# Optimization experiments

Measured on AMD Instinct MI355X. Metric: run time of the kernel, lower is better.

## Reference

```python
import jax, jax.numpy as jnp
import numpy as np

EMBED_DIM = 512
NUM_HEADS = 8
B, L_Q, L_K = 2, 2048, 2048


def setup_inputs() -> dict:
    key = jax.random.key(0)
    ks = jax.random.split(key, 8)
    s = 0.02  # weight init scale
    return {
        "query": jax.random.normal(ks[0], (B, L_Q, EMBED_DIM), jnp.float32),
        "key":   jax.random.normal(ks[1], (B, L_K, EMBED_DIM), jnp.float32),
        "value": jax.random.normal(ks[2], (B, L_K, EMBED_DIM), jnp.float32),
        "wq": jax.random.normal(ks[3], (EMBED_DIM, EMBED_DIM), jnp.float32) * s,
        "wk": jax.random.normal(ks[4], (EMBED_DIM, EMBED_DIM), jnp.float32) * s,
        "wv": jax.random.normal(ks[5], (EMBED_DIM, EMBED_DIM), jnp.float32) * s,
        "bq": jnp.zeros((EMBED_DIM,), jnp.float32),
        "bk": jnp.zeros((EMBED_DIM,), jnp.float32),
        "bv": jnp.zeros((EMBED_DIM,), jnp.float32),
        "wo": jax.random.normal(ks[6], (EMBED_DIM, EMBED_DIM), jnp.float32) * s,
        "bo": jnp.zeros((EMBED_DIM,), jnp.float32),
    }


def _prob_sparse_mask(query, key, num_heads):
    # Faithful to _prob_QK: max-mean sparsity score, top-k query selection,
    # gather of reduced queries, reduced QK matmul (vectorized, no python loops).
    Bq, Lq, D = query.shape
    Lk = key.shape[1]
    dh = D // num_heads
    n_top = int(np.log(Lk))  # int(np.ceil/np.log) as in source forward: int(np.log(L_K))
    Q = query.reshape(Bq, Lq, num_heads, dh)
    K = key.reshape(Bq, Lk, num_heads, dh)
    Qh = jnp.transpose(Q, (0, 2, 1, 3))                      # [B,H,Lq,dh]
    # NOTE: source does K.transpose(1,2).reshape(B,H,D,L_K) -- a reshape, not a
    # transpose of the last two dims. We replicate that exactly.
    Kr = jnp.transpose(K, (0, 2, 1, 3)).reshape(Bq, num_heads, dh, Lk)  # [B,H,dh,Lk]
    QK = jnp.einsum('bhqd,bhdk->bhqk', Qh, Kr)               # [B,H,Lq,Lk]
    M = QK.max(-1) - QK.sum(-1) / Lk                         # max-mean score [B,H,Lq]
    _, M_top = jax.lax.top_k(M, n_top)                       # [B,H,n_top]
    Q_red = jnp.take_along_axis(Qh, M_top[..., None], axis=2)  # [B,H,n_top,dh]
    QK_red = jnp.einsum('bhtd,bhdk->bhtk', Q_red, Kr)        # [B,H,n_top,Lk]
    # Scatter reduced rows back into a full additive attn mask (zeros elsewhere).
    mask = jnp.zeros((Bq, num_heads, Lq, Lk), QK.dtype)
    bi = jnp.arange(Bq)[:, None, None]
    hi = jnp.arange(num_heads)[None, :, None]
    return mask.at[bi, hi, M_top].set(QK_red)


def reference(query, key, value, wq, wk, wv, bq, bk, bv, wo, bo):
    Bq, Lq, D = query.shape
    Lk = key.shape[1]
    H = NUM_HEADS
    dh = D // H
    mask = _prob_sparse_mask(query, key, H)                  # [B,H,Lq,Lk]
    q = (query @ wq.T + bq).reshape(Bq, Lq, H, dh).transpose(0, 2, 1, 3)
    k = (key @ wk.T + bk).reshape(Bq, Lk, H, dh).transpose(0, 2, 1, 3)
    v = (value @ wv.T + bv).reshape(Bq, Lk, H, dh).transpose(0, 2, 1, 3)
    scores = jnp.einsum('bhqd,bhkd->bhqk', q, k) * (dh ** -0.5) + mask
    attn = jax.nn.softmax(scores, axis=-1)                   # dropout inactive (eval)
    out = jnp.einsum('bhqk,bhkd->bhqd', attn, v)
    out = out.transpose(0, 2, 1, 3).reshape(Bq, Lq, D)
    return out @ wo.T + bo
```

## Files before the change

kernel.cpp:

```cpp
#include <hip/hip_runtime.h>
#include <type_traits>

#define DEV static __device__ __forceinline__

typedef short s16;
typedef __attribute__((ext_vector_type(4))) short short4_t;
typedef __attribute__((ext_vector_type(8))) short short8;
typedef __attribute__((ext_vector_type(4))) float f32x4;

#define NB 2
#define NH 8
#define SL 2048
#define DM 512
#define DH 64
#define NTOP 7
#define LOG2E 1.4426950408889634f
#define NROWS (NB*NH*SL)
#define FSPLIT 4
#define SSPLIT 4

DEV short f2bf(float x){
  union { float f; unsigned u; } v; v.f = x;
  unsigned r = v.u + 0x7fffu + ((v.u >> 16) & 1u);
  return (short)(r >> 16);
}
DEV float bf2f(short b){
  union { float f; unsigned u; } v; v.u = ((unsigned)(unsigned short)b) << 16;
  return v.f;
}
DEV f32x4 mfma16(short8 a, short8 b, f32x4 c){
  return __builtin_amdgcn_mfma_f32_16x16x32_bf16(a, b, c, 0, 0, 0);
}
DEV unsigned cvtpk(float lo, float hi){
  unsigned r;
  asm("v_cvt_pk_bf16_f32 %0, %1, %2" : "=v"(r) : "v"(lo), "v"(hi));
  return r;
}
DEV void gl2lds16(const s16* g, s16* l){
  __builtin_amdgcn_global_load_lds(
      (const __attribute__((address_space(1))) unsigned*)g,
      (__attribute__((address_space(3))) unsigned*)l, 16, 0, 0);
}

__global__ void prep_kernel(const float* __restrict__ query, const float* __restrict__ key,
    const float* __restrict__ value,
    const float* __restrict__ wq, const float* __restrict__ wk,
    const float* __restrict__ wv, const float* __restrict__ wo,
    s16* __restrict__ q_hi, s16* __restrict__ q_lo, s16* __restrict__ xk, s16* __restrict__ xv,
    s16* __restrict__ khi, s16* __restrict__ klo,
    s16* __restrict__ wqb, s16* __restrict__ wkb, s16* __restrict__ wvb, s16* __restrict__ wob){
  const int nbb = (NB*SL*DM)/256;
  const int wbb = (DM*DM)/256;
  __shared__ s16 thi[64][66];
  __shared__ s16 tlo[64][66];
  int bid = blockIdx.x;
  int t = threadIdx.x;
  if (bid < nbb){
    int i = bid*256 + t;
    float v = query[i];
    short h = f2bf(v);
    q_hi[i] = h;
    q_lo[i] = f2bf(v - bf2f(h));
    return;
  }
  bid -= nbb;
  if (bid < nbb){ int i = bid*256 + t; xk[i] = f2bf(key[i]); return; }
  bid -= nbb;
  if (bid < nbb){ int i = bid*256 + t; xv[i] = f2bf(value[i]); return; }
  bid -= nbb;
  if (bid < 512){
    int k6 = bid & 31, h = (bid >> 5) & 7, b = bid >> 8;
    int kl = t & 63, dq = t >> 6;
    #pragma unroll
    for (int dd = 0; dd < 16; ++dd){
      int d = dd*4 + dq;
      float v = key[((size_t)b*SL + d*32 + k6)*DM + h*DH + kl];
      short hh = f2bf(v);
      thi[d][kl] = hh;
      tlo[d][kl] = f2bf(v - bf2f(hh));
    }
    __syncthreads();
    int d2 = t & 63, kq = t >> 6;
    size_t obase = (((size_t)(b*NH + h))*SL + (size_t)k6*64)*DH;
    #pragma unroll
    for (int kk = 0; kk < 16; ++kk){
      int kl2 = kk*4 + kq;
      khi[obase + (size_t)kl2*DH + d2] = thi[d2][kl2];
      klo[obase + (size_t)kl2*DH + d2] = tlo[d2][kl2];
    }
    return;
  }
  bid -= 512;
  if (bid < wbb){ int i = bid*256 + t; wqb[i] = f2bf(wq[i]); return; }
  bid -= wbb;
  if (bid < wbb){ int i = bid*256 + t; wkb[i] = f2bf(wk[i]); return; }
  bid -= wbb;
  if (bid < wbb){ int i = bid*256 + t; wvb[i] = f2bf(wv[i]); return; }
  bid -= wbb;
  if (bid < wbb){ int i = bid*256 + t; wob[i] = f2bf(wo[i]); return; }
}

__global__ __launch_bounds__(256) void vpt_kernel(const s16* __restrict__ Vp, s16* __restrict__ VpT){
  __shared__ s16 tl[64][66];
  int bid = blockIdx.x;
  int k6 = bid & 31, h = (bid >> 5) & 7, b = bid >> 8;
  int t = threadIdx.x;
  int d = t & 63, kq = t >> 6;
  #pragma unroll
  for (int kk = 0; kk < 16; ++kk){
    int kl = kk*4 + kq;
    tl[kl][d] = Vp[((size_t)b*SL + k6*64 + kl)*DM + h*DH + d];
  }
  __syncthreads();
  int kl2 = t & 63, dq = t >> 6;
  int kp = (kl2 & 32) + ((kl2 >> 2) & 3)*8 + (kl2 & 3) + ((kl2 >> 4) & 1)*4;
  size_t obase = ((size_t)(b*NH + h))*DH*SL + (size_t)k6*64;
  #pragma unroll
  for (int dd = 0; dd < 16; ++dd){
    int d2 = dd*4 + dq;
    VpT[obase + (size_t)d2*SL + kp] = tl[kl2][d2];
  }
}

template<int OUTF32>
DEV void gemm_body(const s16* __restrict__ A, const s16* __restrict__ Bw,
        const float* __restrict__ bias, void* __restrict__ Cout, int bid, int tid, float scale){
  __shared__ __align__(16) s16 Abuf[2][128*64];
  __shared__ __align__(16) s16 Bbuf[2][64*64];
  int nt = bid >> 3, ot = bid & 7;
  int w = tid >> 6, l = tid & 63;
  int lr = l & 15, lg = l >> 4;
  int n0 = nt*128, o0 = ot*64;
  auto stage = [&](int cur, int kg){
    #pragma unroll
    for (int i = 0; i < 4; ++i){
      int r = w*32 + i*8 + (l>>3);
      int cs = (l&7) ^ (r&7);
      gl2lds16(A + (size_t)(n0 + r)*DM + kg + cs*8, &Abuf[cur][(w*32 + i*8)*64]);
    }
    #pragma unroll
    for (int i = 0; i < 2; ++i){
      int r = w*16 + i*8 + (l>>3);
      int cs = (l&7) ^ (r&7);
      gl2lds16(Bw + (size_t)(o0 + r)*DM + kg + cs*8, &Bbuf[cur][(w*16 + i*8)*64]);
    }
  };
  f32x4 acc[2][4] = {};
  stage(0, 0);
  __syncthreads();
  const int NIT = DM/64;
  for (int it = 0; it < NIT; ++it){
    int cur = it & 1;
    if (it + 1 < NIT) stage(cur^1, (it+1)*64);
    #pragma unroll
    for (int kc = 0; kc < 2; ++kc){
      short8 a0 = *(const short8*)&Abuf[cur][(w*32 +      lr)*64 + ((kc*4+lg) ^ (lr&7))*8];
      short8 a1 = *(const short8*)&Abuf[cur][(w*32 + 16 + lr)*64 + ((kc*4+lg) ^ (lr&7))*8];
      #pragma unroll
      for (int c = 0; c < 4; ++c){
        short8 bf = *(const short8*)&Bbuf[cur][(c*16 + lr)*64 + ((kc*4+lg) ^ (lr&7))*8];
        acc[0][c] = mfma16(a0, bf, acc[0][c]);
        acc[1][c] = mfma16(a1, bf, acc[1][c]);
      }
    }
    __syncthreads();
  }
  #pragma unroll
  for (int sub = 0; sub < 2; ++sub)
    #pragma unroll
    for (int c = 0; c < 4; ++c){
      int col = o0 + c*16 + lr;
      float bb = bias[col];
      #pragma unroll
      for (int j = 0; j < 4; ++j){
        int row = n0 + w*32 + sub*16 + lg*4 + j;
        float v = (acc[sub][c][j] + bb)*scale;
        if (OUTF32) ((float*)Cout)[(size_t)row*DM + col] = v;
        else        ((s16*) Cout)[(size_t)row*DM + col] = f2bf(v);
      }
    }
}

__global__ __launch_bounds__(256) void gemm_proj(const s16* __restrict__ Aq, const s16* __restrict__ Ak,
        const s16* __restrict__ Av, const s16* __restrict__ Wq, const s16* __restrict__ Wk,
        const s16* __restrict__ Wv, const float* __restrict__ bq, const float* __restrict__ bk,
        const float* __restrict__ bv, s16* __restrict__ Oq, s16* __restrict__ Ok, s16* __restrict__ Ov){
  int which = blockIdx.x >> 8;
  const s16* A  = which == 0 ? Aq : which == 1 ? Ak : Av;
  const s16* Bw = which == 0 ? Wq : which == 1 ? Wk : Wv;
  const float* bias = which == 0 ? bq : which == 1 ? bk : bv;
  s16* C = which == 0 ? Oq : which == 1 ? Ok : Ov;
  float scale = which == 0 ? 0.125f*LOG2E : 1.0f;
  gemm_body<0>(A, Bw, bias, C, blockIdx.x & 255, threadIdx.x, scale);
}

__global__ __launch_bounds__(256) void gemm_out(const s16* __restrict__ A, const s16* __restrict__ Bw,
        const float* __restrict__ bias, float* __restrict__ Cout){
  gemm_body<1>(A, Bw, bias, Cout, blockIdx.x, threadIdx.x, 1.0f);
}

__global__ __launch_bounds__(512) void stats_kernel(const s16* __restrict__ qhi, const s16* __restrict__ qlo,
        const s16* __restrict__ khi, const s16* __restrict__ klo,
        float* __restrict__ Mmx, float* __restrict__ Msm){
  __shared__ __align__(16) s16 Hbuf[2][64*64];
  __shared__ __align__(16) s16 Lbuf[2][64*64];
  int bid = blockIdx.x;
  int s = bid & 3, qt = (bid >> 2) & 15, h = (bid >> 6) & 7, b = bid >> 9;
  int tid = threadIdx.x;
  int w = tid >> 6, l = tid & 63;
  int lr = l & 15, lg = l >> 4;
  int dx = lr & 7;
  int q0 = qt*128 + w*16;
  const s16* qp  = qhi + ((size_t)b*SL + q0 + lr)*DM + h*DH + lg*8;
  const s16* qlp = qlo + ((size_t)b*SL + q0 + lr)*DM + h*DH + lg*8;
  short8 qh0 = *(const short8*)qp;
  short8 qh1 = *(const short8*)(qp + 32);
  short8 ql0 = *(const short8*)qlp;
  short8 ql1 = *(const short8*)(qlp + 32);
  const s16* kb  = khi + ((size_t)b*NH + h)*SL*DH;
  const s16* klb = klo + ((size_t)b*NH + h)*SL*DH;
  const s16* hR0 = &Hbuf[0][lr*64 + ((lg      ^ dx)*8)];
  const s16* hR1 = &Hbuf[0][lr*64 + (((4+lg) ^ dx)*8)];
  const s16* lR0 = &Lbuf[0][lr*64 + ((lg      ^ dx)*8)];
  const s16* lR1 = &Lbuf[0][lr*64 + (((4+lg) ^ dx)*8)];
  int rS = tid >> 3;
  int csK = (tid & 7) ^ (rS & 7);
  auto stage = [&](int cur, int kg){
    gl2lds16(kb  + (size_t)(kg + rS)*DH + csK*8, &Hbuf[cur][w*512]);
    gl2lds16(klb + (size_t)(kg + rS)*DH + csK*8, &Lbuf[cur][w*512]);
  };
  float mx = -1e30f, sm = 0.f;
  auto body = [&](auto CURC){
    constexpr int CUR = decltype(CURC)::value;
    #pragma unroll
    for (int t = 0; t < 4; ++t){
      short8 kh0 = *(const short8*)(hR0 + CUR*4096 + t*1024);
      short8 kh1 = *(const short8*)(hR1 + CUR*4096 + t*1024);
      short8 kl0 = *(const short8*)(lR0 + CUR*4096 + t*1024);
      short8 kl1 = *(const short8*)(lR1 + CUR*4096 + t*1024);
      f32x4 sacc = {};
      sacc = mfma16(kh0, qh0, sacc);
      sacc = mfma16(kh1, qh1, sacc);
      sacc = mfma16(kl0, qh0, sacc);
      sacc = mfma16(kl1, qh1, sacc);
      sacc = mfma16(kh0, ql0, sacc);
      sacc = mfma16(kh1, ql1, sacc);
      #pragma unroll
      for (int j = 0; j < 4; ++j){ mx = fmaxf(mx, sacc[j]); sm += sacc[j]; }
    }
  };
  int kbeg = s*(SL/SSPLIT);
  const int NI2 = (SL/SSPLIT)/128;
  stage(0, kbeg);
  __syncthreads();
  #pragma unroll 1
  for (int i2 = 0; i2 < NI2; ++i2){
    stage(1, kbeg + (2*i2+1)*64);
    body(std::integral_constant<int,0>{});
    __syncthreads();
    if (i2 < NI2-1) stage(0, kbeg + (2*i2+2)*64);
    body(std::integral_constant<int,1>{});
    __syncthreads();
  }
  mx = fmaxf(mx, __shfl_xor(mx, 16));
  mx = fmaxf(mx, __shfl_xor(mx, 32));
  sm += __shfl_xor(sm, 16);
  sm += __shfl_xor(sm, 32);
  if (lg == 0){
    size_t row = ((size_t)b*NH + h)*SL + q0 + lr;
    Mmx[(size_t)s*NROWS + row] = mx;
    Msm[(size_t)s*NROWS + row] = sm;
  }
}

__global__ __launch_bounds__(256) void topk_kernel(const float* __restrict__ Mmx,
        const float* __restrict__ Msm, int* __restrict__ topidx, int* __restrict__ rowsel){
  int bh = blockIdx.x;
  int t = threadIdx.x;
  int w = t >> 6, l = t & 63;
  __shared__ float smv[SL];
  __shared__ float rv[4];
  __shared__ int   ri[4];
  size_t base = (size_t)bh*SL;
  for (int i = t; i < SL; i += 256){
    float mx = Mmx[base + i];
    float sm = Msm[base + i];
    #pragma unroll
    for (int s = 1; s < SSPLIT; ++s){
      mx = fmaxf(mx, Mmx[(size_t)s*NROWS + base + i]);
      sm += Msm[(size_t)s*NROWS + base + i];
    }
    smv[i] = mx - sm*(1.0f/SL);
    rowsel[base + i] = -1;
  }
  __syncthreads();
  for (int tt = 0; tt < NTOP; ++tt){
    float bvv = -1e38f; int bi = SL;
    for (int i = t; i < SL; i += 256){
      float v = smv[i];
      if (v > bvv){ bvv = v; bi = i; }
    }
    #pragma unroll
    for (int off = 32; off >= 1; off >>= 1){
      float ov = __shfl_xor(bvv, off);
      int oi = __shfl_xor(bi, off);
      if (ov > bvv || (ov == bvv && oi < bi)){ bvv = ov; bi = oi; }
    }
    if (l == 0){ rv[w] = bvv; ri[w] = bi; }
    __syncthreads();
    if (t == 0){
      float bv2 = rv[0]; int bi2 = ri[0];
      #pragma unroll
      for (int ww = 1; ww < 4; ++ww)
        if (rv[ww] > bv2 || (rv[ww] == bv2 && ri[ww] < bi2)){ bv2 = rv[ww]; bi2 = ri[ww]; }
      topidx[bh*8 + tt] = bi2;
      rowsel[base + bi2] = tt;
      smv[bi2] = -1e38f;
    }
    __syncthreads();
  }
}

__global__ __launch_bounds__(256) void maskrow_kernel(const float* __restrict__ query,
        const float* __restrict__ key, const int* __restrict__ topidx, float* __restrict__ maskrows){
  __shared__ float tile[64][65];
  __shared__ float qs[NTOP][64];
  int bid = blockIdx.x;
  int k6 = bid & 31, h = (bid >> 5) & 7, b = bid >> 8;
  int bh = b*NH + h;
  int t = threadIdx.x;
  int kl = t & 63, w = t >> 6;
  for (int i = t; i < NTOP*64; i += 256){
    int tt = i >> 6, d = i & 63;
    qs[tt][d] = query[((size_t)b*SL + topidx[bh*8 + tt])*DM + h*DH + d];
  }
  #pragma unroll
  for (int dd = 0; dd < 16; ++dd){
    int d = dd*4 + w;
    tile[d][kl] = key[((size_t)b*SL + d*32 + k6)*DM + h*DH + kl];
  }
  __syncthreads();
  for (int tt = w; tt < NTOP; tt += 4){
    float acc = 0.f;
    #pragma unroll
    for (int d = 0; d < 64; ++d)
      acc = fmaf(qs[tt][d], tile[d][kl], acc);
    maskrows[((size_t)bh*NTOP + tt)*SL + k6*64 + kl] = acc*LOG2E;
  }
}

__global__ __launch_bounds__(512) void flash_kernel(const s16* __restrict__ Qp, const s16* __restrict__ Kp,
        const s16* __restrict__ VpT, const float* __restrict__ maskrows, const int* __restrict__ rowsel,
        float* __restrict__ Opart, float* __restrict__ lpart){
  __shared__ __align__(16) s16 Kbuf[2][64*64];
  __shared__ __align__(16) s16 Vbuf[2][64*64];
  int bid = blockIdx.x;
  int s = bid & 3, qt = (bid >> 2) & 15, h = (bid >> 6) & 7, b = bid >> 9;
  int tid = threadIdx.x;
  int w = tid >> 6, l = tid & 63;
  int lr = l & 15, lg = l >> 4;
  int dx = lr & 7;
  int q0 = qt*128 + w*16;
  int bh = b*NH + h;
  const s16* qp = Qp + ((size_t)b*SL + q0 + lr)*DM + h*DH + lg*8;
  short8 bq0 = *(const short8*)qp;
  short8 bq1 = *(const short8*)(qp + 32);
  int sel = rowsel[(size_t)bh*SL + q0 + lr];
  const float* mrow = maskrows + ((size_t)bh*NTOP + (sel >= 0 ? sel : 0))*SL;
  const s16* kpb = Kp + (size_t)b*SL*DM + h*DH;
  const s16* vtb = VpT + (size_t)bh*DH*SL;
  const s16* kR0 = &Kbuf[0][lr*64 + ((lg      ^ dx)*8)];
  const s16* kR1 = &Kbuf[0][lr*64 + (((4+lg) ^ dx)*8)];
  const s16* vR0 = &Vbuf[0][lr*64 + ((lg      ^ dx)*8)];
  const s16* vR1 = &Vbuf[0][lr*64 + (((4+lg) ^ dx)*8)];
  int rS = tid >> 3;
  int csK = (tid & 7) ^ (rS & 7);
  auto stage = [&](int cur, int kg){
    gl2lds16(kpb + (size_t)(kg + rS)*DM + csK*8, &Kbuf[cur][w*512]);
    gl2lds16(vtb + (size_t)rS*SL + kg + csK*8, &Vbuf[cur][w*512]);
  };
  f32x4 acc[4] = {};
  float ls0 = 0.f, ls1 = 0.f, ls2 = 0.f, ls3 = 0.f;
  auto body = [&](auto CURC, int k0){
    constexpr int CUR = decltype(CURC)::value;
    float pv[4][4];
    #pragma unroll
    for (int t = 0; t < 4; ++t){
      short8 ka0 = *(const short8*)(kR0 + CUR*4096 + t*1024);
      short8 ka1 = *(const short8*)(kR1 + CUR*4096 + t*1024);
      f32x4 sc = {};
      sc = mfma16(ka0, bq0, sc);
      sc = mfma16(ka1, bq1, sc);
      #pragma unroll
      for (int j = 0; j < 4; ++j) pv[t][j] = sc[j];
    }
    if (sel >= 0){
      #pragma unroll
      for (int t = 0; t < 4; ++t)
        #pragma unroll
        for (int j = 0; j < 4; ++j)
          pv[t][j] += mrow[k0 + t*16 + lg*4 + j];
    }
    #pragma unroll
    for (int t = 0; t < 4; ++t){
      pv[t][0] = exp2f(pv[t][0]); ls0 += pv[t][0];
      pv[t][1] = exp2f(pv[t][1]); ls1 += pv[t][1];
      pv[t][2] = exp2f(pv[t][2]); ls2 += pv[t][2];
      pv[t][3] = exp2f(pv[t][3]); ls3 += pv[t][3];
    }
    short8 paf[2];
    #pragma unroll
    for (int kt = 0; kt < 2; ++kt){
      union { unsigned u[4]; short8 s8; } uu;
      uu.u[0] = cvtpk(pv[2*kt][0],   pv[2*kt][1]);
      uu.u[1] = cvtpk(pv[2*kt][2],   pv[2*kt][3]);
      uu.u[2] = cvtpk(pv[2*kt+1][0], pv[2*kt+1][1]);
      uu.u[3] = cvtpk(pv[2*kt+1][2], pv[2*kt+1][3]);
      paf[kt] = uu.s8;
    }
    #pragma unroll
    for (int c = 0; c < 4; ++c){
      short8 vf0 = *(const short8*)(vR0 + CUR*4096 + c*1024);
      acc[c] = mfma16(vf0, paf[0], acc[c]);
      short8 vf1 = *(const short8*)(vR1 + CUR*4096 + c*1024);
      acc[c] = mfma16(vf1, paf[1], acc[c]);
    }
  };
  int kbeg = s*(SL/FSPLIT);
  const int NI2 = (SL/FSPLIT)/128;
  stage(0, kbeg);
  __syncthreads();
  #pragma unroll 1
  for (int i2 = 0; i2 < NI2; ++i2){
    stage(1, kbeg + (2*i2+1)*64);
    body(std::integral_constant<int,0>{}, kbeg + 2*i2*64);
    __syncthreads();
    if (i2 < NI2-1) stage(0, kbeg + (2*i2+2)*64);
    body(std::integral_constant<int,1>{}, kbeg + (2*i2+1)*64);
    __syncthreads();
  }
  float lsum = (ls0 + ls1) + (ls2 + ls3);
  lsum += __shfl_xor(lsum, 16);
  lsum += __shfl_xor(lsum, 32);
  size_t row = (size_t)bh*SL + q0 + lr;
  float* Op = Opart + ((size_t)s*NROWS + row)*DH;
  #pragma unroll
  for (int c = 0; c < 4; ++c)
    *(f32x4*)(Op + c*16 + lg*4) = acc[c];
  if (lg == 0)
    lpart[(size_t)s*NROWS + row] = lsum;
}

__global__ __launch_bounds__(256) void flash_combine(const float* __restrict__ Opart,
        const float* __restrict__ lpart, s16* __restrict__ outh){
  int row = blockIdx.x*4 + (threadIdx.x >> 6);
  int d = threadIdx.x & 63;
  float L = 0.f, o = 0.f;
  #pragma unroll
  for (int s = 0; s < FSPLIT; ++s){
    L += lpart[(size_t)s*NROWS + row];
    o += Opart[((size_t)s*NROWS + row)*DH + d];
  }
  o /= L;
  int b = row >> 14, h = (row >> 11) & 7, q = row & (SL - 1);
  outh[((size_t)b*SL + q)*DM + h*DH + d] = f2bf(o);
}

extern "C" void kernel_launch(void* const* d_in, const int* in_sizes, int n_in,
                              void* d_out, int out_size, void* d_ws, size_t ws_size,
                              hipStream_t stream){
  (void)in_sizes; (void)n_in; (void)out_size;
  const float* query = (const float*)d_in[0];
  const float* key   = (const float*)d_in[1];
  const float* value = (const float*)d_in[2];
  const float* wq    = (const float*)d_in[3];
  const float* wk    = (const float*)d_in[4];
  const float* wv    = (const float*)d_in[5];
  const float* bq    = (const float*)d_in[6];
  const float* bk    = (const float*)d_in[7];
  const float* bv    = (const float*)d_in[8];
  const float* wo    = (const float*)d_in[9];
  const float* bo    = (const float*)d_in[10];

  const size_t NE = (size_t)NB*SL*DM;
  const size_t WE = (size_t)DM*DM;

  char* p = (char*)d_ws;
  size_t off = 0;
  auto alloc = [&](size_t n)->char*{ char* r = p + off; off += (n + 255) & ~(size_t)255; return r; };
  s16* wob = (s16*)alloc(WE*2);
  s16* Qp  = (s16*)alloc(NE*2);
  s16* Kp  = (s16*)alloc(NE*2);
  s16* VpT = (s16*)alloc(NE*2);
  float* maskrows = (float*)alloc((size_t)NB*NH*NTOP*SL*4);
  int* topidx   = (int*)alloc((size_t)NB*NH*8*4);
  int* rowsel   = (int*)alloc((size_t)NROWS*4);
  float* Mmx    = (float*)alloc((size_t)SSPLIT*NROWS*4);
  float* Msm    = (float*)alloc((size_t)SSPLIT*NROWS*4);
  float* lpart  = (float*)alloc((size_t)FSPLIT*NROWS*4);
  float* Opart  = (float*)alloc((size_t)FSPLIT*NROWS*DH*4);
  s16* outh = (s16*)alloc(NE*2);
  s16* q_hi = (s16*)alloc(NE*2);
  s16* q_lo = (s16*)alloc(NE*2);
  s16* xk   = (s16*)alloc(NE*2);
  s16* xv   = (s16*)alloc(NE*2);
  s16* khatT_hi = (s16*)alloc(NE*2);
  s16* khatT_lo = (s16*)alloc(NE*2);
  s16* wqb = (s16*)alloc(WE*2);
  s16* wkb = (s16*)alloc(WE*2);
  s16* wvb = (s16*)alloc(WE*2);
  s16* Vp  = (s16*)alloc(NE*2);
  if (off > ws_size) return;

  const int nbb = (int)(NE/256);
  const int wbb = (int)(WE/256);
  prep_kernel<<<3*nbb + 512 + 4*wbb, 256, 0, stream>>>(query, key, value, wq, wk, wv, wo,
      q_hi, q_lo, xk, xv, khatT_hi, khatT_lo, wqb, wkb, wvb, wob);

  gemm_proj<<<3*256, 256, 0, stream>>>(q_hi, xk, xv, wqb, wkb, wvb, bq, bk, bv, Qp, Kp, Vp);
  vpt_kernel<<<512, 256, 0, stream>>>(Vp, VpT);

  stats_kernel<<<NB*NH*(SL/128)*SSPLIT, 512, 0, stream>>>(q_hi, q_lo, khatT_hi, khatT_lo, Mmx, Msm);
  topk_kernel<<<NB*NH, 256, 0, stream>>>(Mmx, Msm, topidx, rowsel);
  maskrow_kernel<<<512, 256, 0, stream>>>(query, key, topidx, maskrows);

  flash_kernel<<<NB*NH*(SL/128)*FSPLIT, 512, 0, stream>>>(Qp, Kp, VpT, maskrows, rowsel,
      Opart, lpart);
  flash_combine<<<NROWS/4, 256, 0, stream>>>(Opart, lpart, outh);
  gemm_out<<<256, 256, 0, stream>>>(outh, wob, bo, (float*)d_out);
}
```

Baseline: 141.3 us.

## Deepen K/V staging to a 4-buffer async pipeline with explicit vmcnt waits

Result: slower. 147.5 us (+4.4%).

```diff
diff --git a/kernel.cpp b/kernel.cpp
--- a/kernel.cpp
+++ b/kernel.cpp
@@ -18,6 +18,10 @@
 #define NROWS (NB*NH*SL)
 #define FSPLIT 4
 #define SSPLIT 4
+
+#define SCHEDB() __builtin_amdgcn_sched_barrier(0)
+#define WAITVM(N) do{ asm volatile("s_waitcnt vmcnt(" #N ")" ::: "memory"); SCHEDB(); }while(0)
+#define BAR() do{ __builtin_amdgcn_s_barrier(); SCHEDB(); }while(0)
 
 DEV short f2bf(float x){
   union { float f; unsigned u; } v; v.f = x;
@@ -202,8 +206,8 @@
 __global__ __launch_bounds__(512) void stats_kernel(const s16* __restrict__ qhi, const s16* __restrict__ qlo,
         const s16* __restrict__ khi, const s16* __restrict__ klo,
         float* __restrict__ Mmx, float* __restrict__ Msm){
-  __shared__ __align__(16) s16 Hbuf[2][64*64];
-  __shared__ __align__(16) s16 Lbuf[2][64*64];
+  __shared__ __align__(16) s16 Hbuf[4][64*64];
+  __shared__ __align__(16) s16 Lbuf[4][64*64];
   int bid = blockIdx.x;
   int s = bid & 3, qt = (bid >> 2) & 15, h = (bid >> 6) & 7, b = bid >> 9;
   int tid = threadIdx.x;
@@ -225,9 +229,10 @@
   const s16* lR1 = &Lbuf[0][lr*64 + (((4+lg) ^ dx)*8)];
   int rS = tid >> 3;
   int csK = (tid & 7) ^ (rS & 7);
-  auto stage = [&](int cur, int kg){
-    gl2lds16(kb  + (size_t)(kg + rS)*DH + csK*8, &Hbuf[cur][w*512]);
-    gl2lds16(klb + (size_t)(kg + rS)*DH + csK*8, &Lbuf[cur][w*512]);
+  int kbeg = s*(SL/SSPLIT);
+  auto stage = [&](int buf, int kg){
+    gl2lds16(kb  + (size_t)(kg + rS)*DH + csK*8, &Hbuf[buf][w*512]);
+    gl2lds16(klb + (size_t)(kg + rS)*DH + csK*8, &Lbuf[buf][w*512]);
   };
   float mx = -1e30f, sm = 0.f;
   auto body = [&](auto CURC){
@@ -249,19 +254,24 @@
       for (int j = 0; j < 4; ++j){ mx = fmaxf(mx, sacc[j]); sm += sacc[j]; }
     }
   };
-  int kbeg = s*(SL/SSPLIT);
-  const int NI2 = (SL/SSPLIT)/128;
-  stage(0, kbeg);
-  __syncthreads();
-  #pragma unroll 1
-  for (int i2 = 0; i2 < NI2; ++i2){
-    stage(1, kbeg + (2*i2+1)*64);
-    body(std::integral_constant<int,0>{});
-    __syncthreads();
-    if (i2 < NI2-1) stage(0, kbeg + (2*i2+2)*64);
-    body(std::integral_constant<int,1>{});
-    __syncthreads();
-  }
+  stage(0, kbeg); stage(1, kbeg + 64); stage(2, kbeg + 128);
+  auto step = [&](auto TC){
+    constexpr int T = decltype(TC)::value;
+    BAR();
+    if constexpr (T + 3 < 8) stage((T+3)&3, kbeg + (T+3)*64);
+    if constexpr (T <= 4) WAITVM(6);
+    else if constexpr (T == 5) WAITVM(4);
+    else if constexpr (T == 6) WAITVM(2);
+    else WAITVM(0);
+    BAR();
+    __builtin_amdgcn_s_setprio(1);
+    body(std::integral_constant<int, T&3>{});
+    __builtin_amdgcn_s_setprio(0);
+  };
+  step(std::integral_constant<int,0>{}); step(std::integral_constant<int,1>{});
+  step(std::integral_constant<int,2>{}); step(std::integral_constant<int,3>{});
+  step(std::integral_constant<int,4>{}); step(std::integral_constant<int,5>{});
+  step(std::integral_constant<int,6>{}); step(std::integral_constant<int,7>{});
   mx = fmaxf(mx, __shfl_xor(mx, 16));
   mx = fmaxf(mx, __shfl_xor(mx, 32));
   sm += __shfl_xor(sm, 16);
@@ -352,8 +362,8 @@
 __global__ __launch_bounds__(512) void flash_kernel(const s16* __restrict__ Qp, const s16* __restrict__ Kp,
         const s16* __restrict__ VpT, const float* __restrict__ maskrows, const int* __restrict__ rowsel,
         float* __restrict__ Opart, float* __restrict__ lpart){
-  __shared__ __align__(16) s16 Kbuf[2][64*64];
-  __shared__ __align__(16) s16 Vbuf[2][64*64];
+  __shared__ __align__(16) s16 Kbuf[4][64*64];
+  __shared__ __align__(16) s16 Vbuf[4][64*64];
   int bid = blockIdx.x;
   int s = bid & 3, qt = (bid >> 2) & 15, h = (bid >> 6) & 7, b = bid >> 9;
   int tid = threadIdx.x;
@@ -375,9 +385,10 @@
   const s16* vR1 = &Vbuf[0][lr*64 + (((4+lg) ^ dx)*8)];
   int rS = tid >> 3;
   int csK = (tid & 7) ^ (rS & 7);
-  auto stage = [&](int cur, int kg){
-    gl2lds16(kpb + (size_t)(kg + rS)*DM + csK*8, &Kbuf[cur][w*512]);
-    gl2lds16(vtb + (size_t)rS*SL + kg + csK*8, &Vbuf[cur][w*512]);
+  int kbeg = s*(SL/FSPLIT);
+  auto stage = [&](int buf, int kg){
+    gl2lds16(kpb + (size_t)(kg + rS)*DM + csK*8, &Kbuf[buf][w*512]);
+    gl2lds16(vtb + (size_t)rS*SL + kg + csK*8, &Vbuf[buf][w*512]);
   };
   f32x4 acc[4] = {};
   float ls0 = 0.f, ls1 = 0.f, ls2 = 0.f, ls3 = 0.f;
@@ -426,19 +437,24 @@
       acc[c] = mfma16(vf1, paf[1], acc[c]);
     }
   };
-  int kbeg = s*(SL/FSPLIT);
-  const int NI2 = (SL/FSPLIT)/128;
-  stage(0, kbeg);
-  __syncthreads();
-  #pragma unroll 1
-  for (int i2 = 0; i2 < NI2; ++i2){
-    stage(1, kbeg + (2*i2+1)*64);
-    body(std::integral_constant<int,0>{}, kbeg + 2*i2*64);
-    __syncthreads();
-    if (i2 < NI2-1) stage(0, kbeg + (2*i2+2)*64);
-    body(std::integral_constant<int,1>{}, kbeg + (2*i2+1)*64);
-    __syncthreads();
-  }
+  stage(0, kbeg); stage(1, kbeg + 64); stage(2, kbeg + 128);
+  auto step = [&](auto TC){
+    constexpr int T = decltype(TC)::value;
+    BAR();
+    if constexpr (T + 3 < 8) stage((T+3)&3, kbeg + (T+3)*64);
+    if constexpr (T <= 4) WAITVM(6);
+    else if constexpr (T == 5) WAITVM(4);
+    else if constexpr (T == 6) WAITVM(2);
+    else WAITVM(0);
+    BAR();
+    __builtin_amdgcn_s_setprio(1);
+    body(std::integral_constant<int, T&3>{}, kbeg + T*64);
+    __builtin_amdgcn_s_setprio(0);
+  };
+  step(std::integral_constant<int,0>{}); step(std::integral_constant<int,1>{});
+  step(std::integral_constant<int,2>{}); step(std::integral_constant<int,3>{});
+  step(std::integral_constant<int,4>{}); step(std::integral_constant<int,5>{});
+  step(std::integral_constant<int,6>{}); step(std::integral_constant<int,7>{});
   float lsum = (ls0 + ls1) + (ls2 + ls3);
   lsum += __shfl_xor(lsum, 16);
   lsum += __shfl_xor(lsum, 32);
```

## Switch flash attention to 32x32x16 MFMA with 4 waves of 32 rows

Applied to the files above, without the earlier changes.

Result: no change. 140.2 us (-0.7%).

```diff
diff --git a/kernel.cpp b/kernel.cpp
--- a/kernel.cpp
+++ b/kernel.cpp
@@ -7,6 +7,7 @@
 typedef __attribute__((ext_vector_type(4))) short short4_t;
 typedef __attribute__((ext_vector_type(8))) short short8;
 typedef __attribute__((ext_vector_type(4))) float f32x4;
+typedef __attribute__((ext_vector_type(16))) float f32x16;
 
 #define NB 2
 #define NH 8
@@ -30,6 +31,9 @@
 }
 DEV f32x4 mfma16(short8 a, short8 b, f32x4 c){
   return __builtin_amdgcn_mfma_f32_16x16x32_bf16(a, b, c, 0, 0, 0);
+}
+DEV f32x16 mfma32(short8 a, short8 b, f32x16 c){
+  return __builtin_amdgcn_mfma_f32_32x32x16_bf16(a, b, c, 0, 0, 0);
 }
 DEV unsigned cvtpk(float lo, float hi){
   unsigned r;
@@ -113,12 +117,11 @@
   }
   __syncthreads();
   int kl2 = t & 63, dq = t >> 6;
-  int kp = (kl2 & 32) + ((kl2 >> 2) & 3)*8 + (kl2 & 3) + ((kl2 >> 4) & 1)*4;
   size_t obase = ((size_t)(b*NH + h))*DH*SL + (size_t)k6*64;
   #pragma unroll
   for (int dd = 0; dd < 16; ++dd){
     int d2 = dd*4 + dq;
-    VpT[obase + (size_t)d2*SL + kp] = tl[kl2][d2];
+    VpT[obase + (size_t)d2*SL + kl2] = tl[kl2][d2];
   }
 }
 
@@ -349,82 +352,97 @@
   }
 }
 
-__global__ __launch_bounds__(512) void flash_kernel(const s16* __restrict__ Qp, const s16* __restrict__ Kp,
-        const s16* __restrict__ VpT, const float* __restrict__ maskrows, const int* __restrict__ rowsel,
+__global__ __launch_bounds__(256, 3) void flash_kernel(const s16* __restrict__ Qp,
+        const s16* __restrict__ Kp, const s16* __restrict__ VpT,
+        const float* __restrict__ maskrows, const int* __restrict__ rowsel,
         float* __restrict__ Opart, float* __restrict__ lpart){
-  __shared__ __align__(16) s16 Kbuf[2][64*64];
-  __shared__ __align__(16) s16 Vbuf[2][64*64];
+  __shared__ __align__(16) s16 SB[4*64*64];
   int bid = blockIdx.x;
   int s = bid & 3, qt = (bid >> 2) & 15, h = (bid >> 6) & 7, b = bid >> 9;
   int tid = threadIdx.x;
   int w = tid >> 6, l = tid & 63;
-  int lr = l & 15, lg = l >> 4;
-  int dx = lr & 7;
-  int q0 = qt*128 + w*16;
+  int ln = l & 31, lh = l >> 5;
+  int q0 = qt*128 + w*32;
   int bh = b*NH + h;
-  const s16* qp = Qp + ((size_t)b*SL + q0 + lr)*DM + h*DH + lg*8;
-  short8 bq0 = *(const short8*)qp;
-  short8 bq1 = *(const short8*)(qp + 32);
-  int sel = rowsel[(size_t)bh*SL + q0 + lr];
+  const s16* qp = Qp + ((size_t)b*SL + q0 + ln)*DM + h*DH + lh*8;
+  short8 bq[4];
+  #pragma unroll
+  for (int kc = 0; kc < 4; ++kc) bq[kc] = *(const short8*)(qp + kc*16);
+  int sel = rowsel[(size_t)bh*SL + q0 + ln];
   const float* mrow = maskrows + ((size_t)bh*NTOP + (sel >= 0 ? sel : 0))*SL;
   const s16* kpb = Kp + (size_t)b*SL*DM + h*DH;
   const s16* vtb = VpT + (size_t)bh*DH*SL;
-  const s16* kR0 = &Kbuf[0][lr*64 + ((lg      ^ dx)*8)];
-  const s16* kR1 = &Kbuf[0][lr*64 + (((4+lg) ^ dx)*8)];
-  const s16* vR0 = &Vbuf[0][lr*64 + ((lg      ^ dx)*8)];
-  const s16* vR1 = &Vbuf[0][lr*64 + (((4+lg) ^ dx)*8)];
-  int rS = tid >> 3;
-  int csK = (tid & 7) ^ (rS & 7);
+  const s16* kR[2][4];
+  #pragma unroll
+  for (int g = 0; g < 2; ++g)
+    #pragma unroll
+    for (int kc = 0; kc < 4; ++kc)
+      kR[g][kc] = &SB[(g*32 + ln)*64 + (((kc*2 + lh) ^ (ln & 7))*8)];
+  int rS8 = l >> 3;
+  int csS = (l & 7) ^ (rS8 & 7);
   auto stage = [&](int cur, int kg){
-    gl2lds16(kpb + (size_t)(kg + rS)*DM + csK*8, &Kbuf[cur][w*512]);
-    gl2lds16(vtb + (size_t)rS*SL + kg + csK*8, &Vbuf[cur][w*512]);
+    #pragma unroll
+    for (int c = 0; c < 2; ++c){
+      int r = c*32 + w*8 + rS8;
+      gl2lds16(kpb + (size_t)(kg + r)*DM + csS*8, &SB[(size_t)cur*4096 + (c*32 + w*8)*64]);
+      gl2lds16(vtb + (size_t)r*SL + kg + csS*8, &SB[8192 + (size_t)cur*4096 + (c*32 + w*8)*64]);
+    }
   };
-  f32x4 acc[4] = {};
+  f32x16 accO[2] = {};
   float ls0 = 0.f, ls1 = 0.f, ls2 = 0.f, ls3 = 0.f;
   auto body = [&](auto CURC, int k0){
-    constexpr int CUR = decltype(CURC)::value;
-    float pv[4][4];
-    #pragma unroll
-    for (int t = 0; t < 4; ++t){
-      short8 ka0 = *(const short8*)(kR0 + CUR*4096 + t*1024);
-      short8 ka1 = *(const short8*)(kR1 + CUR*4096 + t*1024);
-      f32x4 sc = {};
-      sc = mfma16(ka0, bq0, sc);
-      sc = mfma16(ka1, bq1, sc);
-      #pragma unroll
-      for (int j = 0; j < 4; ++j) pv[t][j] = sc[j];
-    }
+    constexpr int CB = decltype(CURC)::value * 8192;
+    f32x16 S[2] = {};
+    #pragma unroll
+    for (int g = 0; g < 2; ++g)
+      #pragma unroll
+      for (int kc = 0; kc < 4; ++kc){
+        short8 kf = *(const short8*)((const char*)kR[g][kc] + CB);
+        S[g] = mfma32(kf, bq[kc], S[g]);
+      }
     if (sel >= 0){
       #pragma unroll
-      for (int t = 0; t < 4; ++t)
+      for (int g = 0; g < 2; ++g)
         #pragma unroll
-        for (int j = 0; j < 4; ++j)
-          pv[t][j] += mrow[k0 + t*16 + lg*4 + j];
-    }
-    #pragma unroll
-    for (int t = 0; t < 4; ++t){
-      pv[t][0] = exp2f(pv[t][0]); ls0 += pv[t][0];
-      pv[t][1] = exp2f(pv[t][1]); ls1 += pv[t][1];
-      pv[t][2] = exp2f(pv[t][2]); ls2 += pv[t][2];
-      pv[t][3] = exp2f(pv[t][3]); ls3 += pv[t][3];
-    }
-    short8 paf[2];
-    #pragma unroll
-    for (int kt = 0; kt < 2; ++kt){
+        for (int rq = 0; rq < 4; ++rq)
+          #pragma unroll
+          for (int j = 0; j < 4; ++j)
+            S[g][rq*4 + j] += mrow[k0 + g*32 + rq*8 + lh*4 + j];
+    }
+    #pragma unroll
+    for (int g = 0; g < 2; ++g)
+      #pragma unroll
+      for (int rq = 0; rq < 4; ++rq){
+        S[g][rq*4+0] = exp2f(S[g][rq*4+0]); ls0 += S[g][rq*4+0];
+        S[g][rq*4+1] = exp2f(S[g][rq*4+1]); ls1 += S[g][rq*4+1];
+        S[g][rq*4+2] = exp2f(S[g][rq*4+2]); ls2 += S[g][rq*4+2];
+        S[g][rq*4+3] = exp2f(S[g][rq*4+3]); ls3 += S[g][rq*4+3];
+      }
+    unsigned W[2][8];
+    #pragma unroll
+    for (int g = 0; g < 2; ++g)
+      #pragma unroll
+      for (int t = 0; t < 8; ++t)
+        W[g][t] = cvtpk(S[g][2*t], S[g][2*t+1]);
+    short8 pf[4];
+    #pragma unroll
+    for (int kc = 0; kc < 4; ++kc){
+      int g = kc >> 1, j = kc & 1;
+      unsigned a0 = W[g][4*j + 0], a1 = W[g][4*j + 2];
+      asm("v_permlane32_swap_b32 %0, %1" : "+v"(a0), "+v"(a1));
+      unsigned b0 = W[g][4*j + 1], b1 = W[g][4*j + 3];
+      asm("v_permlane32_swap_b32 %0, %1" : "+v"(b0), "+v"(b1));
       union { unsigned u[4]; short8 s8; } uu;
-      uu.u[0] = cvtpk(pv[2*kt][0],   pv[2*kt][1]);
-      uu.u[1] = cvtpk(pv[2*kt][2],   pv[2*kt][3]);
-      uu.u[2] = cvtpk(pv[2*kt+1][0], pv[2*kt+1][1]);
-      uu.u[3] = cvtpk(pv[2*kt+1][2], pv[2*kt+1][3]);
-      paf[kt] = uu.s8;
-    }
-    #pragma unroll
-    for (int c = 0; c < 4; ++c){
-      short8 vf0 = *(const short8*)(vR0 + CUR*4096 + c*1024);
-      acc[c] = mfma16(vf0, paf[0], acc[c]);
-      short8 vf1 = *(const short8*)(vR1 + CUR*4096 + c*1024);
-      acc[c] = mfma16(vf1, paf[1], acc[c]);
-    }
+      uu.u[0] = a0; uu.u[1] = b0; uu.u[2] = a1; uu.u[3] = b1;
+      pf[kc] = uu.s8;
+    }
+    #pragma unroll
+    for (int dg = 0; dg < 2; ++dg)
+      #pragma unroll
+      for (int kc = 0; kc < 4; ++kc){
+        short8 vf = *(const short8*)((const char*)kR[dg][kc] + CB + 16384);
+        accO[dg] = mfma32(vf, pf[kc], accO[dg]);
+      }
   };
   int kbeg = s*(SL/FSPLIT);
   const int NI2 = (SL/FSPLIT)/128;
@@ -440,14 +458,17 @@
     __syncthreads();
   }
   float lsum = (ls0 + ls1) + (ls2 + ls3);
-  lsum += __shfl_xor(lsum, 16);
   lsum += __shfl_xor(lsum, 32);
-  size_t row = (size_t)bh*SL + q0 + lr;
+  size_t row = (size_t)bh*SL + q0 + ln;
   float* Op = Opart + ((size_t)s*NROWS + row)*DH;
   #pragma unroll
-  for (int c = 0; c < 4; ++c)
-    *(f32x4*)(Op + c*16 + lg*4) = acc[c];
-  if (lg == 0)
+  for (int dg = 0; dg < 2; ++dg)
+    #pragma unroll
+    for (int rq = 0; rq < 4; ++rq){
+      f32x4 v = { accO[dg][rq*4+0], accO[dg][rq*4+1], accO[dg][rq*4+2], accO[dg][rq*4+3] };
+      *(f32x4*)(Op + dg*32 + rq*8 + lh*4) = v;
+    }
+  if (lh == 0)
     lpart[(size_t)s*NROWS + row] = lsum;
 }
 
@@ -524,7 +545,7 @@
   topk_kernel<<<NB*NH, 256, 0, stream>>>(Mmx, Msm, topidx, rowsel);
   maskrow_kernel<<<512, 256, 0, stream>>>(query, key, topidx, maskrows);
 
-  flash_kernel<<<NB*NH*(SL/128)*FSPLIT, 512, 0, stream>>>(Qp, Kp, VpT, maskrows, rowsel,
+  flash_kernel<<<NB*NH*(SL/128)*FSPLIT, 256, 0, stream>>>(Qp, Kp, VpT, maskrows, rowsel,
       Opart, lpart);
   flash_combine<<<NROWS/4, 256, 0, stream>>>(Opart, lpart, outh);
   gemm_out<<<256, 256, 0, stream>>>(outh, wob, bo, (float*)d_out);
```
